# Kernel tuning notes

Measured on AMD Instinct MI355X. Metric: run time of the kernel, lower is better.

The kernel has to match this reference:

```python
import jax, jax.numpy as jnp
import numpy as np

B, T, F, H, A, DFF, DEMO, NH = 64, 96, 48, 128, 8, 512, 12, 4
DM = H  # d_model == hidden_dim


def _linear(x, W, b):
    # torch nn.Linear: y = x @ W.T + b, W: [out, in]
    return jnp.einsum('...i,oi->...o', x, W) + b


def _layernorm(x, a, b, eps=1e-7):
    # matches the custom LayerNorm: unbiased std (torch.std default)
    mean = x.mean(-1, keepdims=True)
    std = jnp.std(x, axis=-1, keepdims=True, ddof=1)
    return a * (x - mean) / (std + eps) + b


def _forward(x, demo, gru_Wih, gru_Whh, gru_bih, gru_bhh, att_Wt, att_Wx, att_rate,
             demoW, demob, mWq, mbq, mWk, mbk, mWv, mbv, mWo, mbo,
             ln1_a, ln1_b, ln2_a, ln2_b, ffn_W1, ffn_b1, ffn_W2, ffn_b2,
             fWq, fbq, fWk, fbk, fWv, fbv, outW, outb):
    Bs, Ts, Fs = x.shape
    Hd = gru_Whh.shape[-1]

    # ---- per-feature GRUs (input size 1), vectorized over the F features ----
    def step(h, xt):  # h: [B,F,H], xt: [B,F]
        gi = xt[:, :, None] * gru_Wih[None] + gru_bih[None]            # [B,F,3H]
        gh = jnp.einsum('bfh,fgh->bfg', h, gru_Whh) + gru_bhh[None]    # [B,F,3H]
        ir, iz, inn = jnp.split(gi, 3, -1)
        hr, hz, hn = jnp.split(gh, 3, -1)
        r = jax.nn.sigmoid(ir + hr)
        z = jax.nn.sigmoid(iz + hz)
        n = jnp.tanh(inn + r * hn)
        hnew = (1.0 - z) * n + z * h
        return hnew, hnew

    h0 = jnp.zeros((Bs, Fs, Hd), x.dtype)
    _, Hs = jax.lax.scan(step, h0, jnp.moveaxis(x, 1, 0))  # [T,B,F,H]
    Hs = jnp.moveaxis(Hs, 0, 1)                            # [B,T,F,H]

    # ---- time-aware per-feature attention (SingleAttentionPerFeatureNew) ----
    q = jnp.einsum('bfh,fha->bfa', Hs[:, -1], att_Wt)      # query from last step
    k = jnp.einsum('btfh,fha->btfa', Hs, att_Wx)
    dot = jnp.einsum('bfa,btfa->btf', q, k)                # [B,T,F]
    b_time = jnp.arange(Ts, 0, -1, dtype=x.dtype)[None, :, None]  # T..1
    sr = jax.nn.sigmoid(att_rate)[None, None, :]
    sd = jax.nn.sigmoid(dot)
    denom = sr * (jnp.log(2.72 + (1.0 - sd)) * b_time)
    e = jax.nn.relu(sd / denom)
    a = jax.nn.softmax(e, axis=1)                          # softmax over time
    v = jnp.einsum('btf,btfh->bfh', a, Hs)                 # [B,F,H]

    # ---- demographics channel + concat ----
    demo_main = jnp.tanh(_linear(demo, demoW, demob))[:, None, :]
    posi = jnp.concatenate([v, demo_main], axis=1)         # [B,F+1,H]

    # ---- MHA sublayer (pre-norm residual) with DeCov ----
    xn = _layernorm(posi, ln1_a, ln1_b)
    N = xn.shape[1]
    dk = DM // NH
    qh = _linear(xn, mWq, mbq).reshape(Bs, N, NH, dk).transpose(0, 2, 1, 3)
    kh = _linear(xn, mWk, mbk).reshape(Bs, N, NH, dk).transpose(0, 2, 1, 3)
    vh = _linear(xn, mWv, mbv).reshape(Bs, N, NH, dk).transpose(0, 2, 1, 3)
    scores = jnp.einsum('bhnd,bhmd->bhnm', qh, kh) / jnp.sqrt(jnp.asarray(dk, x.dtype))
    p = jax.nn.softmax(scores, axis=-1)
    ctx = jnp.einsum('bhnm,bhmd->bhnd', p, vh).transpose(0, 2, 1, 3).reshape(Bs, N, DM)
    mha_out = _linear(ctx, mWo, mbo)                       # [B,N,DM]

    # DeCov loss: per position n, covariance across batch, off-diagonal Frobenius
    xc = mha_out - mha_out.mean(axis=0, keepdims=True)     # center over batch
    cov = jnp.einsum('bnh,bng->nhg', xc, xc) / (Bs - 1.0)  # [N,H,H]
    diag = jnp.diagonal(cov, axis1=1, axis2=2)             # [N,H]
    decov = 0.5 * (jnp.sum(cov * cov) - jnp.sum(diag * diag))

    h1 = posi + mha_out

    # ---- FFN sublayer (pre-norm residual) ----
    xn2 = _layernorm(h1, ln2_a, ln2_b)
    ffn = _linear(jax.nn.relu(_linear(xn2, ffn_W1, ffn_b1)), ffn_W2, ffn_b2)
    h2 = h1 + ffn

    # ---- FinalAttentionQKV, attention_type='mul' ----
    fq = _linear(h2[:, -1, :], fWq, fbq)                   # [B,DM]
    fk = _linear(h2, fWk, fbk)                             # [B,N,DM]
    fv = _linear(h2, fWv, fbv)
    fe = jnp.einsum('bna,ba->bn', fk, fq)
    alpha = jax.nn.softmax(fe, axis=1)
    pooled = jnp.einsum('bn,bna->ba', alpha, fv)

    out = jax.nn.sigmoid(_linear(pooled, outW, outb))      # [B,1]
    return out, decov


def setup_inputs() -> dict:
    key = jax.random.key(0)
    ks = jax.random.split(key, 40)
    f32 = jnp.float32

    def rn(k, shape, s=0.05):
        return jax.random.normal(k, shape, dtype=f32) * s

    return {
        'x': jax.random.normal(ks[0], (B, T, F), dtype=f32),
        'demo': jax.random.normal(ks[1], (B, DEMO), dtype=f32),
        'gru_Wih': rn(ks[2], (F, 3 * H)),
        'gru_Whh': rn(ks[3], (F, 3 * H, H)),
        'gru_bih': rn(ks[4], (F, 3 * H)),
        'gru_bhh': rn(ks[5], (F, 3 * H)),
        'att_Wt': rn(ks[6], (F, H, A)),
        'att_Wx': rn(ks[7], (F, H, A)),
        'att_rate': jnp.full((F,), 0.8, dtype=f32),
        'demoW': rn(ks[8], (H, DEMO)), 'demob': rn(ks[9], (H,)),
        'mWq': rn(ks[10], (DM, DM)), 'mbq': rn(ks[11], (DM,)),
        'mWk': rn(ks[12], (DM, DM)), 'mbk': rn(ks[13], (DM,)),
        'mWv': rn(ks[14], (DM, DM)), 'mbv': rn(ks[15], (DM,)),
        'mWo': rn(ks[16], (DM, DM)), 'mbo': rn(ks[17], (DM,)),
        'ln1_a': jnp.ones((DM,), dtype=f32), 'ln1_b': jnp.zeros((DM,), dtype=f32),
        'ln2_a': jnp.ones((DM,), dtype=f32), 'ln2_b': jnp.zeros((DM,), dtype=f32),
        'ffn_W1': rn(ks[18], (DFF, DM)), 'ffn_b1': rn(ks[19], (DFF,)),
        'ffn_W2': rn(ks[20], (DM, DFF)), 'ffn_b2': rn(ks[21], (DM,)),
        'fWq': rn(ks[22], (DM, DM)), 'fbq': rn(ks[23], (DM,)),
        'fWk': rn(ks[24], (DM, DM)), 'fbk': rn(ks[25], (DM,)),
        'fWv': rn(ks[26], (DM, DM)), 'fbv': rn(ks[27], (DM,)),
        'outW': rn(ks[28], (1, DM)), 'outb': rn(ks[29], (1,)),
    }


def reference(x, demo, gru_Wih, gru_Whh, gru_bih, gru_bhh, att_Wt, att_Wx, att_rate,
              demoW, demob, mWq, mbq, mWk, mbk, mWv, mbv, mWo, mbo,
              ln1_a, ln1_b, ln2_a, ln2_b, ffn_W1, ffn_b1, ffn_W2, ffn_b2,
              fWq, fbq, fWk, fbk, fWv, fbv, outW, outb):
    return _forward(x, demo, gru_Wih, gru_Whh, gru_bih, gru_bhh, att_Wt, att_Wx, att_rate,
                    demoW, demob, mWq, mbq, mWk, mbk, mWv, mbv, mWo, mbo,
                    ln1_a, ln1_b, ln2_a, ln2_b, ffn_W1, ffn_b1, ffn_W2, ffn_b2,
                    fWq, fbq, fWk, fbk, fWv, fbv, outW, outb)
```

## Files before the change

### kernel.cpp

```cpp
#include <hip/hip_runtime.h>
#include <hip/hip_bf16.h>

namespace {

constexpr int Bc = 64, Tc = 96, Fc = 48, Hc = 128, Ac = 8;
constexpr int DFFc = 512, DEMOc = 12, NHc = 4, Nc = 49, H3c = 384, DKc = 32;

typedef __attribute__((ext_vector_type(8))) short s8v;
typedef __attribute__((ext_vector_type(4))) float f4v;
typedef __attribute__((ext_vector_type(4))) short s4v;

__device__ __forceinline__ float sigf(float x) { return 1.f / (1.f + expf(-x)); }
__device__ __forceinline__ float sigf_fast(float x) { return 1.f / (1.f + __expf(-x)); }
__device__ __forceinline__ float tanhf_fast(float x) {
  float e = __expf(2.f * x);
  return 1.f - 2.f / (e + 1.f);
}

__device__ __forceinline__ unsigned short f2b(float v) {
  __hip_bfloat16 h = __float2bfloat16(v);
  union { __hip_bfloat16 b; unsigned short u; } c;
  c.b = h;
  return c.u;
}
__device__ __forceinline__ float b2f(unsigned short u) {
  union { unsigned u32; float f; } c;
  c.u32 = (unsigned)u << 16;
  return c.f;
}

template <typename ST> __device__ __forceinline__ void stv(ST* p, float v);
template <> __device__ __forceinline__ void stv<float>(float* p, float v) { *p = v; }
template <> __device__ __forceinline__ void stv<__hip_bfloat16>(__hip_bfloat16* p, float v) {
  *p = __float2bfloat16(v);
}

template <typename ST> __device__ __forceinline__ void ld4(const ST* p, float* o);
template <> __device__ __forceinline__ void ld4<float>(const float* p, float* o) {
  float4 v = *reinterpret_cast<const float4*>(p);
  o[0] = v.x; o[1] = v.y; o[2] = v.z; o[3] = v.w;
}
template <> __device__ __forceinline__ void ld4<__hip_bfloat16>(const __hip_bfloat16* p, float* o) {
  ushort4 v = *reinterpret_cast<const ushort4*>(p);
  union { unsigned u; float f; } t;
  t.u = (unsigned)v.x << 16; o[0] = t.f;
  t.u = (unsigned)v.y << 16; o[1] = t.f;
  t.u = (unsigned)v.z << 16; o[2] = t.f;
  t.u = (unsigned)v.w << 16; o[3] = t.f;
}

__device__ __forceinline__ float bsum(float v, float* red, int nw) {
#pragma unroll
  for (int off = 32; off > 0; off >>= 1) v += __shfl_down(v, off);
  int lane = threadIdx.x & 63, wid = threadIdx.x >> 6;
  __syncthreads();
  if (lane == 0) red[wid] = v;
  __syncthreads();
  float s = 0.f;
  for (int i = 0; i < nw; i++) s += red[i];
  return s;
}

template <typename ST>
__global__ __launch_bounds__(512, 2) void gru_mfma(
    const float* __restrict__ x, const float* __restrict__ Wih,
    const float* __restrict__ Whh, const float* __restrict__ bih,
    const float* __restrict__ bhh, ST* __restrict__ Hs, float* __restrict__ hT) {
  const int f = blockIdx.x;
  const int b0 = blockIdx.y << 4;
  const int tid = threadIdx.x;
  const int lane = tid & 63;
  const int w = tid >> 6;
  const int hh = (w << 4) + (lane & 15);
  const int lg = lane >> 4;

  s8v wh[12], wl[12];
#pragma unroll
  for (int gate = 0; gate < 3; gate++) {
#pragma unroll
    for (int ks = 0; ks < 4; ks++) {
      const float* wp = Whh + ((size_t)f * H3c + gate * Hc + hh) * Hc + (ks << 5) + (lg << 3);
      s8v hi, lo;
#pragma unroll
      for (int j = 0; j < 8; j++) {
        float v = wp[j];
        unsigned short hb = f2b(v);
        unsigned short lb = f2b(v - b2f(hb));
        hi[j] = (short)hb;
        lo[j] = (short)lb;
      }
      wh[gate * 4 + ks] = hi;
      wl[gate * 4 + ks] = lo;
    }
  }

  const float wi0 = Wih[f * H3c + hh], wi1 = Wih[f * H3c + Hc + hh], wi2 = Wih[f * H3c + 2 * Hc + hh];
  const float bi0 = bih[f * H3c + hh], bi1 = bih[f * H3c + Hc + hh], bi2 = bih[f * H3c + 2 * Hc + hh];
  const float bh0 = bhh[f * H3c + hh], bh1 = bhh[f * H3c + Hc + hh], bh2 = bhh[f * H3c + 2 * Hc + hh];

  __shared__ unsigned short hbuf[2][2][16 * 128];
  __shared__ float xs[16][100];

  {
    unsigned short* hz = &hbuf[0][0][0];
    for (int i = tid; i < 2 * 2 * 16 * 128; i += 512) hz[i] = 0;
    for (int i = tid; i < 16 * Tc; i += 512) {
      int b = i / Tc, t = i - b * Tc;
      xs[b][t] = x[((size_t)(b0 + b) * Tc + t) * Fc + f];
    }
  }
  __syncthreads();

  float hold[4] = {0.f, 0.f, 0.f, 0.f};
  int cur = 0;

  for (int t = 0; t < Tc; t++) {
    s8v ahi[4], alo[4];
#pragma unroll
    for (int ks = 0; ks < 4; ks++) {
      int m = lane & 15;
      int idx = m * 128 + ((((ks << 2) + lg) ^ (m & 7)) << 3);
      ahi[ks] = *reinterpret_cast<const s8v*>(&hbuf[cur][0][idx]);
      alo[ks] = *reinterpret_cast<const s8v*>(&hbuf[cur][1][idx]);
    }
    f4v accr = {0.f, 0.f, 0.f, 0.f}, accz = {0.f, 0.f, 0.f, 0.f}, accn = {0.f, 0.f, 0.f, 0.f};
#pragma unroll
    for (int ks = 0; ks < 4; ks++) {
      accr = __builtin_amdgcn_mfma_f32_16x16x32_bf16(ahi[ks], wh[0 + ks], accr, 0, 0, 0);
      accz = __builtin_amdgcn_mfma_f32_16x16x32_bf16(ahi[ks], wh[4 + ks], accz, 0, 0, 0);
      accn = __builtin_amdgcn_mfma_f32_16x16x32_bf16(ahi[ks], wh[8 + ks], accn, 0, 0, 0);
      accr = __builtin_amdgcn_mfma_f32_16x16x32_bf16(alo[ks], wh[0 + ks], accr, 0, 0, 0);
      accz = __builtin_amdgcn_mfma_f32_16x16x32_bf16(alo[ks], wh[4 + ks], accz, 0, 0, 0);
      accn = __builtin_amdgcn_mfma_f32_16x16x32_bf16(alo[ks], wh[8 + ks], accn, 0, 0, 0);
      accr = __builtin_amdgcn_mfma_f32_16x16x32_bf16(ahi[ks], wl[0 + ks], accr, 0, 0, 0);
      accz = __builtin_amdgcn_mfma_f32_16x16x32_bf16(ahi[ks], wl[4 + ks], accz, 0, 0, 0);
      accn = __builtin_amdgcn_mfma_f32_16x16x32_bf16(ahi[ks], wl[8 + ks], accn, 0, 0, 0);
    }
    int nxt = cur ^ 1;
#pragma unroll
    for (int r = 0; r < 4; r++) {
      int bt = (lg << 2) + r;
      float xv = xs[bt][t];
      float rr = sigf_fast(xv * wi0 + bi0 + accr[r] + bh0);
      float zz = sigf_fast(xv * wi1 + bi1 + accz[r] + bh1);
      float nn = tanhf_fast(xv * wi2 + bi2 + rr * (accn[r] + bh2));
      float hn = (1.f - zz) * nn + zz * hold[r];
      hold[r] = hn;
      stv(&Hs[(((size_t)(b0 + bt) * Tc + t) * Fc + f) * Hc + hh], hn);
      unsigned short hb = f2b(hn);
      unsigned short lb = f2b(hn - b2f(hb));
      int widx = bt * 128 + (((hh >> 3) ^ (bt & 7)) << 3) + (hh & 7);
      hbuf[nxt][0][widx] = hb;
      hbuf[nxt][1][widx] = lb;
    }
    cur = nxt;
    __syncthreads();
  }
#pragma unroll
  for (int r = 0; r < 4; r++) {
    int bt = (lg << 2) + r;
    hT[((size_t)(b0 + bt) * Fc + f) * Hc + hh] = hold[r];
  }
}

template <typename ST>
__global__ __launch_bounds__(256) void feat_attn(
    const ST* __restrict__ Hs, const float* __restrict__ hT,
    const float* __restrict__ Wt, const float* __restrict__ Wx,
    const float* __restrict__ rate, float* __restrict__ posi) {
  const int f = blockIdx.x, b = blockIdx.y;
  const int tid = threadIdx.x;
  __shared__ float tile[Tc][Hc + 1];
  __shared__ float wxs[Hc][Ac];
  __shared__ float qs[Ac];
  __shared__ float es[Tc];
  __shared__ float red[2];

  for (int i = tid; i < Tc * (Hc / 4); i += 256) {
    int t = i >> 5, k = (i & 31) << 2;
    float o[4];
    ld4(&Hs[(((size_t)b * Tc + t) * Fc + f) * Hc + k], o);
    tile[t][k] = o[0]; tile[t][k + 1] = o[1]; tile[t][k + 2] = o[2]; tile[t][k + 3] = o[3];
  }
  for (int i = tid; i < Hc * Ac; i += 256) (&wxs[0][0])[i] = Wx[(size_t)f * Hc * Ac + i];
  if (tid < Ac) {
    float q = 0.f;
    const float* hTp = hT + ((size_t)b * Fc + f) * Hc;
    for (int h = 0; h < Hc; h++) q += hTp[h] * Wt[((size_t)f * Hc + h) * Ac + tid];
    qs[tid] = q;
  }
  __syncthreads();
  if (tid < Tc) {
    float ka[Ac];
#pragma unroll
    for (int a = 0; a < Ac; a++) ka[a] = 0.f;
    for (int h = 0; h < Hc; h++) {
      float hv = tile[tid][h];
#pragma unroll
      for (int a = 0; a < Ac; a++) ka[a] += hv * wxs[h][a];
    }
    float dot = 0.f;
#pragma unroll
    for (int a = 0; a < Ac; a++) dot += qs[a] * ka[a];
    float sd = sigf(dot);
    float denom = sigf(rate[f]) * (logf(2.72f + (1.f - sd)) * (float)(Tc - tid));
    es[tid] = fmaxf(sd / denom, 0.f);
  }
  __syncthreads();
  if (tid == 0) {
    float m = -1e30f;
    for (int t = 0; t < Tc; t++) m = fmaxf(m, es[t]);
    red[0] = m;
  }
  __syncthreads();
  if (tid < Tc) es[tid] = expf(es[tid] - red[0]);
  __syncthreads();
  if (tid == 0) {
    float s = 0.f;
    for (int t = 0; t < Tc; t++) s += es[t];
    red[1] = 1.f / s;
  }
  __syncthreads();
  if (tid < Hc) {
    float acc = 0.f;
    for (int t = 0; t < Tc; t++) acc += es[t] * tile[t][tid];
    posi[((size_t)b * Nc + f) * Hc + tid] = acc * red[1];
  }
}

__global__ __launch_bounds__(128) void demo_k(
    const float* __restrict__ demo, const float* __restrict__ dW,
    const float* __restrict__ db, float* __restrict__ posi) {
  int b = blockIdx.x, h = threadIdx.x;
  float acc = db[h];
  const float* dp = demo + b * DEMOc;
  const float* wp = dW + h * DEMOc;
#pragma unroll
  for (int d = 0; d < DEMOc; d++) acc += dp[d] * wp[d];
  posi[((size_t)b * Nc + (Nc - 1)) * Hc + h] = tanhf(acc);
}

__global__ __launch_bounds__(128) void ln_qkv(
    const float* __restrict__ posi, const float* __restrict__ ga, const float* __restrict__ be,
    const float* __restrict__ Wq, const float* __restrict__ bq,
    const float* __restrict__ Wk, const float* __restrict__ bk,
    const float* __restrict__ Wv, const float* __restrict__ bv,
    float* __restrict__ qb, float* __restrict__ kb, float* __restrict__ vb) {
  int bn = blockIdx.x;
  int b = bn / Nc, n = bn % Nc;
  int h = threadIdx.x;
  __shared__ float xn[Hc];
  __shared__ float red[2];
  float xv = posi[(size_t)bn * Hc + h];
  float m = bsum(xv, red, 2) * (1.f / Hc);
  float d = xv - m;
  float var = bsum(d * d, red, 2) * (1.f / (Hc - 1));
  xn[h] = ga[h] * d / (sqrtf(var) + 1e-7f) + be[h];
  __syncthreads();
  float q = bq[h], k = bk[h], v = bv[h];
  for (int kk = 0; kk < Hc; kk++) {
    float xk = xn[kk];
    q += xk * Wq[h * Hc + kk];
    k += xk * Wk[h * Hc + kk];
    v += xk * Wv[h * Hc + kk];
  }
  int head = h >> 5, dd = h & 31;
  size_t o = (((size_t)b * NHc + head) * Nc + n) * DKc + dd;
  qb[o] = q; kb[o] = k; vb[o] = v;
}

__global__ __launch_bounds__(64) void mha_attn(
    const float* __restrict__ qb, const float* __restrict__ kb,
    const float* __restrict__ vb, float* __restrict__ ctx) {
  int hd = blockIdx.x, b = blockIdx.y;
  int tid = threadIdx.x;
  __shared__ float ksm[Nc][DKc];
  __shared__ float vsm[Nc][DKc];
  __shared__ float sc[Nc][Nc];
  size_t base = ((size_t)b * NHc + hd) * Nc * DKc;
  for (int i = tid; i < Nc * DKc; i += 64) {
    ksm[i / DKc][i % DKc] = kb[base + i];
    vsm[i / DKc][i % DKc] = vb[base + i];
  }
  __syncthreads();
  if (tid < Nc) {
    float qr[DKc];
#pragma unroll
    for (int d = 0; d < DKc; d++) qr[d] = qb[base + tid * DKc + d];
    float mx = -1e30f;
    for (int mm = 0; mm < Nc; mm++) {
      float s = 0.f;
#pragma unroll
      for (int d = 0; d < DKc; d++) s += qr[d] * ksm[mm][d];
      s *= 0.17677669529663687f;
      sc[tid][mm] = s;
      mx = fmaxf(mx, s);
    }
    float ssum = 0.f;
    for (int mm = 0; mm < Nc; mm++) {
      float e = expf(sc[tid][mm] - mx);
      sc[tid][mm] = e;
      ssum += e;
    }
    float inv = 1.f / ssum;
    float acc[DKc];
#pragma unroll
    for (int d = 0; d < DKc; d++) acc[d] = 0.f;
    for (int mm = 0; mm < Nc; mm++) {
      float p = sc[tid][mm] * inv;
#pragma unroll
      for (int d = 0; d < DKc; d++) acc[d] += p * vsm[mm][d];
    }
    float* cp = ctx + ((size_t)b * Nc + tid) * Hc + hd * DKc;
#pragma unroll
    for (int d = 0; d < DKc; d++) cp[d] = acc[d];
  }
}

__global__ __launch_bounds__(128) void wo_res(
    const float* __restrict__ ctx, const float* __restrict__ Wo,
    const float* __restrict__ bo, const float* __restrict__ posi,
    float* __restrict__ mha, float* __restrict__ h1) {
  int bn = blockIdx.x;
  int h = threadIdx.x;
  __shared__ float cs[Hc];
  cs[h] = ctx[(size_t)bn * Hc + h];
  __syncthreads();
  float acc = bo[h];
  for (int k = 0; k < Hc; k++) acc += cs[k] * Wo[h * Hc + k];
  mha[(size_t)bn * Hc + h] = acc;
  h1[(size_t)bn * Hc + h] = posi[(size_t)bn * Hc + h] + acc;
}

__global__ __launch_bounds__(256) void decov_k(
    const float* __restrict__ mha, float* __restrict__ dacc) {
  int n = blockIdx.x;
  int tid = threadIdx.x;
  __shared__ float xc[Bc][Hc];
  __shared__ float red[4];
  for (int i = tid; i < Bc * Hc; i += 256) {
    int b = i >> 7, h = i & 127;
    xc[b][h] = mha[((size_t)b * Nc + n) * Hc + h];
  }
  __syncthreads();
  if (tid < Hc) {
    float s = 0.f;
    for (int b = 0; b < Bc; b++) s += xc[b][tid];
    s *= (1.f / Bc);
    for (int b = 0; b < Bc; b++) xc[b][tid] -= s;
  }
  __syncthreads();
  float p2 = 0.f, pd = 0.f;
  for (int e = tid; e < Hc * Hc; e += 256) {
    int hh = e >> 7, gg = e & 127;
    float c = 0.f;
    for (int b = 0; b < Bc; b++) c += xc[b][hh] * xc[b][gg];
    c *= (1.f / (Bc - 1));
    float c2 = c * c;
    p2 += c2;
    if (hh == gg) pd += c2;
  }
  float s2 = bsum(p2, red, 4);
  float sdg = bsum(pd, red, 4);
  if (tid == 0) atomicAdd(dacc, 0.5f * (s2 - sdg));
}

__global__ __launch_bounds__(256) void ln2_ffn1(
    const float* __restrict__ h1, const float* __restrict__ ga, const float* __restrict__ be,
    const float* __restrict__ W1, const float* __restrict__ b1, float* __restrict__ t1) {
  int bn = blockIdx.x;
  int tid = threadIdx.x;
  __shared__ float xn[Hc];
  __shared__ float red[4];
  float xv = (tid < Hc) ? h1[(size_t)bn * Hc + tid] : 0.f;
  float m = bsum(xv, red, 4) * (1.f / Hc);
  float d = (tid < Hc) ? (xv - m) : 0.f;
  float var = bsum(d * d, red, 4) * (1.f / (Hc - 1));
  if (tid < Hc) xn[tid] = ga[tid] * d / (sqrtf(var) + 1e-7f) + be[tid];
  __syncthreads();
#pragma unroll
  for (int jj = 0; jj < 2; jj++) {
    int j = tid + jj * 256;
    float acc = b1[j];
    for (int k = 0; k < Hc; k++) acc += xn[k] * W1[j * Hc + k];
    t1[(size_t)bn * DFFc + j] = fmaxf(acc, 0.f);
  }
}

__global__ __launch_bounds__(128) void ffn2_res(
    const float* __restrict__ t1, const float* __restrict__ W2,
    const float* __restrict__ b2, const float* __restrict__ h1, float* __restrict__ h2) {
  int bn = blockIdx.x;
  int h = threadIdx.x;
  __shared__ float ts[DFFc];
  for (int i = h; i < DFFc; i += 128) ts[i] = t1[(size_t)bn * DFFc + i];
  __syncthreads();
  float acc = b2[h];
  for (int j = 0; j < DFFc; j++) acc += ts[j] * W2[h * DFFc + j];
  h2[(size_t)bn * Hc + h] = h1[(size_t)bn * Hc + h] + acc;
}

__global__ __launch_bounds__(128) void final_k(
    const float* __restrict__ h2,
    const float* __restrict__ Wq, const float* __restrict__ bq,
    const float* __restrict__ Wk, const float* __restrict__ bk,
    const float* __restrict__ Wv, const float* __restrict__ bv,
    const float* __restrict__ oW, const float* __restrict__ ob,
    const float* __restrict__ dacc, float* __restrict__ out) {
  int b = blockIdx.x, h = threadIdx.x;
  __shared__ float h2s[Nc][Hc];
  __shared__ float fks[Nc][Hc + 1];
  __shared__ float fqs[Hc];
  __shared__ float alphas[Nc];
  __shared__ float red[2];
  __shared__ float r2[2];
  for (int i = h; i < Nc * Hc; i += 128) h2s[i / Hc][i % Hc] = h2[(size_t)b * Nc * Hc + i];
  __syncthreads();
  {
    float q = bq[h];
    for (int k = 0; k < Hc; k++) q += h2s[Nc - 1][k] * Wq[h * Hc + k];
    fqs[h] = q;
  }
  for (int n = 0; n < Nc; n++) {
    float fk = bk[h];
    for (int k = 0; k < Hc; k++) fk += h2s[n][k] * Wk[h * Hc + k];
    fks[n][h] = fk;
  }
  __syncthreads();
  if (h < Nc) {
    float fe = 0.f;
    for (int k = 0; k < Hc; k++) fe += fks[h][k] * fqs[k];
    alphas[h] = fe;
  }
  __syncthreads();
  if (h == 0) {
    float m = -1e30f;
    for (int n = 0; n < Nc; n++) m = fmaxf(m, alphas[n]);
    float s = 0.f;
    for (int n = 0; n < Nc; n++) {
      float e = expf(alphas[n] - m);
      alphas[n] = e;
      s += e;
    }
    red[0] = 1.f / s;
  }
  __syncthreads();
  float inv = red[0];
  float pv = 0.f;
  for (int n = 0; n < Nc; n++) {
    float fv = bv[h];
    for (int k = 0; k < Hc; k++) fv += h2s[n][k] * Wv[h * Hc + k];
    pv += alphas[n] * fv;
  }
  pv *= inv;
  float c = pv * oW[h];
#pragma unroll
  for (int off = 32; off > 0; off >>= 1) c += __shfl_down(c, off);
  int lane = h & 63, wid = h >> 6;
  if (lane == 0) r2[wid] = c;
  __syncthreads();
  if (h == 0) {
    out[b] = sigf(r2[0] + r2[1] + ob[0]);
    if (b == 0) out[Bc] = dacc[0];
  }
}

}

extern "C" void kernel_launch(void* const* d_in, const int* in_sizes, int n_in,
                              void* d_out, int out_size, void* d_ws, size_t ws_size,
                              hipStream_t stream) {
  const float* x    = (const float*)d_in[0];
  const float* demo = (const float*)d_in[1];
  const float* gWih = (const float*)d_in[2];
  const float* gWhh = (const float*)d_in[3];
  const float* gbih = (const float*)d_in[4];
  const float* gbhh = (const float*)d_in[5];
  const float* aWt  = (const float*)d_in[6];
  const float* aWx  = (const float*)d_in[7];
  const float* aRt  = (const float*)d_in[8];
  const float* dW   = (const float*)d_in[9];
  const float* db   = (const float*)d_in[10];
  const float* mWq  = (const float*)d_in[11];
  const float* mbq  = (const float*)d_in[12];
  const float* mWk  = (const float*)d_in[13];
  const float* mbk  = (const float*)d_in[14];
  const float* mWv  = (const float*)d_in[15];
  const float* mbv  = (const float*)d_in[16];
  const float* mWo  = (const float*)d_in[17];
  const float* mbo  = (const float*)d_in[18];
  const float* l1a  = (const float*)d_in[19];
  const float* l1b  = (const float*)d_in[20];
  const float* l2a  = (const float*)d_in[21];
  const float* l2b  = (const float*)d_in[22];
  const float* fW1  = (const float*)d_in[23];
  const float* fb1  = (const float*)d_in[24];
  const float* fW2  = (const float*)d_in[25];
  const float* fb2  = (const float*)d_in[26];
  const float* fWq  = (const float*)d_in[27];
  const float* fbq  = (const float*)d_in[28];
  const float* fWk  = (const float*)d_in[29];
  const float* fbk  = (const float*)d_in[30];
  const float* fWv  = (const float*)d_in[31];
  const float* fbv  = (const float*)d_in[32];
  const float* oW   = (const float*)d_in[33];
  const float* ob   = (const float*)d_in[34];

  char* base = (char*)d_ws;
  size_t off = 0;
  auto take = [&](size_t nfloats) -> float* {
    float* r = (float*)(base + off);
    off += ((nfloats * sizeof(float)) + 255) & ~(size_t)255;
    return r;
  };
  float* dec  = take(64);
  float* hT   = take((size_t)Bc * Fc * Hc);
  float* posi = take((size_t)Bc * Nc * Hc);
  float* qb   = take((size_t)Bc * Nc * Hc);
  float* kb   = take((size_t)Bc * Nc * Hc);
  float* vb   = take((size_t)Bc * Nc * Hc);
  float* ctx  = take((size_t)Bc * Nc * Hc);
  float* mha  = take((size_t)Bc * Nc * Hc);
  float* h1   = take((size_t)Bc * Nc * Hc);
  float* t1   = take((size_t)Bc * Nc * DFFc);
  float* h2   = take((size_t)Bc * Nc * Hc);
  size_t HsElems = (size_t)Bc * Tc * Fc * Hc;
  void* HsPtr = (void*)(base + off);
  bool f32path = (ws_size >= off + HsElems * sizeof(float));

  hipMemsetAsync(dec, 0, sizeof(float), stream);

  dim3 gGru(Fc, Bc / 16);
  dim3 gAtt(Fc, Bc);
  if (f32path) {
    gru_mfma<float><<<gGru, 512, 0, stream>>>(x, gWih, gWhh, gbih, gbhh, (float*)HsPtr, hT);
    feat_attn<float><<<gAtt, 256, 0, stream>>>((const float*)HsPtr, hT, aWt, aWx, aRt, posi);
  } else {
    gru_mfma<__hip_bfloat16><<<gGru, 512, 0, stream>>>(x, gWih, gWhh, gbih, gbhh,
                                                       (__hip_bfloat16*)HsPtr, hT);
    feat_attn<__hip_bfloat16><<<gAtt, 256, 0, stream>>>((const __hip_bfloat16*)HsPtr, hT,
                                                        aWt, aWx, aRt, posi);
  }
  demo_k<<<Bc, 128, 0, stream>>>(demo, dW, db, posi);
  ln_qkv<<<Bc * Nc, 128, 0, stream>>>(posi, l1a, l1b, mWq, mbq, mWk, mbk, mWv, mbv, qb, kb, vb);
  mha_attn<<<dim3(NHc, Bc), 64, 0, stream>>>(qb, kb, vb, ctx);
  wo_res<<<Bc * Nc, 128, 0, stream>>>(ctx, mWo, mbo, posi, mha, h1);
  decov_k<<<Nc, 256, 0, stream>>>(mha, dec);
  ln2_ffn1<<<Bc * Nc, 256, 0, stream>>>(h1, l2a, l2b, fW1, fb1, t1);
  ffn2_res<<<Bc * Nc, 128, 0, stream>>>(t1, fW2, fb2, h1, h2);
  final_k<<<Bc, 128, 0, stream>>>(h2, fWq, fbq, fWk, fbk, fWv, fbv, oW, ob, dec, (float*)d_out);
}
```

Before: 894.2 us.

## Split final attention into per-token K/V projection kernel and reduction kernel

The final stage used to run as one kernel with only 64 blocks, each computing Q, K and V projections for all 49 tokens serially. It is now two kernels. The first spreads the K/V (and last-token Q) projections over 64*49 blocks, and the second does the softmax and weighted sum using wave-shuffle dot products. The decov kernel also moves to 512 threads per block. This adds extra global-memory round trips for the K and V buffers and one more kernel launch, in exchange for much higher parallelism.

```diff
diff --git a/kernel.cpp b/kernel.cpp
--- a/kernel.cpp
+++ b/kernel.cpp
@@ -8,7 +8,6 @@
 
 typedef __attribute__((ext_vector_type(8))) short s8v;
 typedef __attribute__((ext_vector_type(4))) float f4v;
-typedef __attribute__((ext_vector_type(4))) short s4v;
 
 __device__ __forceinline__ float sigf(float x) { return 1.f / (1.f + expf(-x)); }
 __device__ __forceinline__ float sigf_fast(float x) { return 1.f / (1.f + __expf(-x)); }
@@ -332,13 +331,13 @@
   h1[(size_t)bn * Hc + h] = posi[(size_t)bn * Hc + h] + acc;
 }
 
-__global__ __launch_bounds__(256) void decov_k(
+__global__ __launch_bounds__(512) void decov_k(
     const float* __restrict__ mha, float* __restrict__ dacc) {
   int n = blockIdx.x;
   int tid = threadIdx.x;
   __shared__ float xc[Bc][Hc];
-  __shared__ float red[4];
-  for (int i = tid; i < Bc * Hc; i += 256) {
+  __shared__ float red[8];
+  for (int i = tid; i < Bc * Hc; i += 512) {
     int b = i >> 7, h = i & 127;
     xc[b][h] = mha[((size_t)b * Nc + n) * Hc + h];
   }
@@ -351,7 +350,7 @@
   }
   __syncthreads();
   float p2 = 0.f, pd = 0.f;
-  for (int e = tid; e < Hc * Hc; e += 256) {
+  for (int e = tid; e < Hc * Hc; e += 512) {
     int hh = e >> 7, gg = e & 127;
     float c = 0.f;
     for (int b = 0; b < Bc; b++) c += xc[b][hh] * xc[b][gg];
@@ -360,8 +359,8 @@
     p2 += c2;
     if (hh == gg) pd += c2;
   }
-  float s2 = bsum(p2, red, 4);
-  float sdg = bsum(pd, red, 4);
+  float s2 = bsum(p2, red, 8);
+  float sdg = bsum(pd, red, 8);
   if (tid == 0) atomicAdd(dacc, 0.5f * (s2 - sdg));
 }
 
@@ -400,63 +399,76 @@
   h2[(size_t)bn * Hc + h] = h1[(size_t)bn * Hc + h] + acc;
 }
 
-__global__ __launch_bounds__(128) void final_k(
+__global__ __launch_bounds__(128) void final_fkv(
     const float* __restrict__ h2,
-    const float* __restrict__ Wq, const float* __restrict__ bq,
     const float* __restrict__ Wk, const float* __restrict__ bk,
     const float* __restrict__ Wv, const float* __restrict__ bv,
+    const float* __restrict__ Wq, const float* __restrict__ bq,
+    float* __restrict__ fkb, float* __restrict__ fvb, float* __restrict__ fqb) {
+  int bn = blockIdx.x;
+  int b = bn / Nc, n = bn - b * Nc;
+  int h = threadIdx.x;
+  __shared__ float xs[Hc];
+  xs[h] = h2[(size_t)bn * Hc + h];
+  __syncthreads();
+  float k = bk[h], v = bv[h];
+  const float* wkp = Wk + h * Hc;
+  const float* wvp = Wv + h * Hc;
+  for (int kk = 0; kk < Hc; kk++) {
+    float xv = xs[kk];
+    k += xv * wkp[kk];
+    v += xv * wvp[kk];
+  }
+  fkb[(size_t)bn * Hc + h] = k;
+  fvb[(size_t)bn * Hc + h] = v;
+  if (n == Nc - 1) {
+    float q = bq[h];
+    const float* wqp = Wq + h * Hc;
+    for (int kk = 0; kk < Hc; kk++) q += xs[kk] * wqp[kk];
+    fqb[(size_t)b * Hc + h] = q;
+  }
+}
+
+__global__ __launch_bounds__(128) void final2(
+    const float* __restrict__ fkb, const float* __restrict__ fvb,
+    const float* __restrict__ fqb,
     const float* __restrict__ oW, const float* __restrict__ ob,
     const float* __restrict__ dacc, float* __restrict__ out) {
   int b = blockIdx.x, h = threadIdx.x;
-  __shared__ float h2s[Nc][Hc];
-  __shared__ float fks[Nc][Hc + 1];
+  int lane = h & 63, wid = h >> 6;
   __shared__ float fqs[Hc];
   __shared__ float alphas[Nc];
   __shared__ float red[2];
   __shared__ float r2[2];
-  for (int i = h; i < Nc * Hc; i += 128) h2s[i / Hc][i % Hc] = h2[(size_t)b * Nc * Hc + i];
-  __syncthreads();
-  {
-    float q = bq[h];
-    for (int k = 0; k < Hc; k++) q += h2s[Nc - 1][k] * Wq[h * Hc + k];
-    fqs[h] = q;
-  }
-  for (int n = 0; n < Nc; n++) {
-    float fk = bk[h];
-    for (int k = 0; k < Hc; k++) fk += h2s[n][k] * Wk[h * Hc + k];
-    fks[n][h] = fk;
-  }
-  __syncthreads();
-  if (h < Nc) {
-    float fe = 0.f;
-    for (int k = 0; k < Hc; k++) fe += fks[h][k] * fqs[k];
-    alphas[h] = fe;
+  fqs[h] = fqb[(size_t)b * Hc + h];
+  __syncthreads();
+  for (int n = wid; n < Nc; n += 2) {
+    const float* fkp = fkb + ((size_t)b * Nc + n) * Hc;
+    float s = fkp[lane] * fqs[lane] + fkp[lane + 64] * fqs[lane + 64];
+#pragma unroll
+    for (int off = 32; off > 0; off >>= 1) s += __shfl_down(s, off);
+    if (lane == 0) alphas[n] = s;
   }
   __syncthreads();
   if (h == 0) {
     float m = -1e30f;
     for (int n = 0; n < Nc; n++) m = fmaxf(m, alphas[n]);
-    float s = 0.f;
+    float ssum = 0.f;
     for (int n = 0; n < Nc; n++) {
       float e = expf(alphas[n] - m);
       alphas[n] = e;
-      s += e;
-    }
-    red[0] = 1.f / s;
+      ssum += e;
+    }
+    red[0] = 1.f / ssum;
   }
   __syncthreads();
   float inv = red[0];
   float pv = 0.f;
-  for (int n = 0; n < Nc; n++) {
-    float fv = bv[h];
-    for (int k = 0; k < Hc; k++) fv += h2s[n][k] * Wv[h * Hc + k];
-    pv += alphas[n] * fv;
-  }
+  for (int n = 0; n < Nc; n++) pv += alphas[n] * fvb[((size_t)b * Nc + n) * Hc + h];
   pv *= inv;
   float c = pv * oW[h];
 #pragma unroll
   for (int off = 32; off > 0; off >>= 1) c += __shfl_down(c, off);
-  int lane = h & 63, wid = h >> 6;
   if (lane == 0) r2[wid] = c;
   __syncthreads();
   if (h == 0) {
@@ -524,6 +536,9 @@
   float* h1   = take((size_t)Bc * Nc * Hc);
   float* t1   = take((size_t)Bc * Nc * DFFc);
   float* h2   = take((size_t)Bc * Nc * Hc);
+  float* fkb  = take((size_t)Bc * Nc * Hc);
+  float* fvb  = take((size_t)Bc * Nc * Hc);
+  float* fqb  = take((size_t)Bc * Hc);
   size_t HsElems = (size_t)Bc * Tc * Fc * Hc;
   void* HsPtr = (void*)(base + off);
   bool f32path = (ws_size >= off + HsElems * sizeof(float));
@@ -545,8 +560,9 @@
   ln_qkv<<<Bc * Nc, 128, 0, stream>>>(posi, l1a, l1b, mWq, mbq, mWk, mbk, mWv, mbv, qb, kb, vb);
   mha_attn<<<dim3(NHc, Bc), 64, 0, stream>>>(qb, kb, vb, ctx);
   wo_res<<<Bc * Nc, 128, 0, stream>>>(ctx, mWo, mbo, posi, mha, h1);
-  decov_k<<<Nc, 256, 0, stream>>>(mha, dec);
+  decov_k<<<Nc, 512, 0, stream>>>(mha, dec);
   ln2_ffn1<<<Bc * Nc, 256, 0, stream>>>(h1, l2a, l2b, fW1, fb1, t1);
   ffn2_res<<<Bc * Nc, 128, 0, stream>>>(t1, fW2, fb2, h1, h2);
-  final_k<<<Bc, 128, 0, stream>>>(h2, fWq, fbq, fWk, fbk, fWv, fbv, oW, ob, dec, (float*)d_out);
-}
+  final_fkv<<<Bc * Nc, 128, 0, stream>>>(h2, fWk, fbk, fWv, fbv, fWq, fbq, fkb, fvb, fqb);
+  final2<<<Bc, 128, 0, stream>>>(fkb, fvb, fqb, oW, ob, dec, (float*)d_out);
+}
```

Result: faster. 773.2 us (-13.5%).
